# Kernel optimization log

Measured on AMD Instinct MI355X. Metric: run time of the kernel, lower is better.

## Reference

```python
import jax, jax.numpy as jnp
import numpy as np

N = 50000
E = 800000
DIMS = [128, 256, 64, 256, 128]  # encoder 128->256->64, decoder 64->256->128
NEG_SLOPE = 0.01


def setup_inputs() -> dict:
    key = jax.random.key(0)
    keys = jax.random.split(key, 2 + 3 * 4)
    inp = {
        "x": jax.random.normal(keys[0], (N, DIMS[0]), dtype=jnp.float32),
        "edge_index": jax.random.randint(keys[1], (2, E), 0, N, dtype=jnp.int64),
    }
    for i in range(4):
        d_in, d_out = DIMS[i], DIMS[i + 1]
        s = 1.0 / np.sqrt(d_in)
        inp[f"W_rel{i}"] = jax.random.uniform(keys[2 + 3 * i], (d_out, d_in), jnp.float32, -s, s)
        inp[f"W_root{i}"] = jax.random.uniform(keys[3 + 3 * i], (d_out, d_in), jnp.float32, -s, s)
        inp[f"b{i}"] = jax.random.uniform(keys[4 + 3 * i], (d_out,), jnp.float32, -s, s)
    return inp


def graph_conv(x, edge_index, W_rel, W_root, b):
    # PyG GraphConv: lin_rel(sum_{j->i} x_j) + lin_root(x_i), bias in lin_rel
    src, dst = edge_index[0], edge_index[1]
    agg = jax.ops.segment_sum(x[src], dst, num_segments=N)  # [N, d_in]
    return agg @ W_rel.T + b + x @ W_root.T


def reference(x, edge_index,
              W_rel0, W_root0, b0, W_rel1, W_root1, b1,
              W_rel2, W_root2, b2, W_rel3, W_root3, b3):
    params = [(W_rel0, W_root0, b0), (W_rel1, W_root1, b1),
              (W_rel2, W_root2, b2), (W_rel3, W_root3, b3)]
    h = x
    emb = None
    for i, (Wr, Ws, b) in enumerate(params):
        h = graph_conv(h, edge_index, Wr, Ws, b)
        h = jax.nn.leaky_relu(h, negative_slope=NEG_SLOPE)
        if i == 1:  # end of encoder -> embedding
            emb = h
    return h, emb
```

## Files before the change

### kernel.cpp

```cpp
#include <hip/hip_runtime.h>

#define NNODES 50000
#define NCB 196

typedef __attribute__((ext_vector_type(8))) short bf16x8;
typedef __attribute__((ext_vector_type(4))) float f32x4;

__device__ inline short f2bf(float f) {
    unsigned u = __float_as_uint(f);
    unsigned r = (u + 0x7FFFu + ((u >> 16) & 1u)) >> 16;
    return (short)r;
}
__device__ inline float bf2f(short s) {
    return __uint_as_float(((unsigned)(unsigned short)s) << 16);
}
__device__ inline float2 bfp2f(int p) {
    float2 f;
    f.x = __uint_as_float((unsigned)p << 16);
    f.y = __uint_as_float((unsigned)p & 0xFFFF0000u);
    return f;
}
__device__ inline void addbf4(float4& a, int2 v) {
    float2 lo = bfp2f(v.x), hi = bfp2f(v.y);
    a.x += lo.x; a.y += lo.y; a.z += hi.x; a.w += hi.y;
}
__device__ inline void addbf8(float* a, int4 v) {
    float2 l0 = bfp2f(v.x), l1 = bfp2f(v.y), l2 = bfp2f(v.z), l3 = bfp2f(v.w);
    a[0] += l0.x; a[1] += l0.y; a[2] += l1.x; a[3] += l1.y;
    a[4] += l2.x; a[5] += l2.y; a[6] += l3.x; a[7] += l3.y;
}
__device__ inline int pack2(float a, float b) {
    return ((int)(unsigned short)f2bf(a)) | ((int)f2bf(b) << 16);
}

__device__ inline int excl_scan_256(int v, int* lds, int tid) {
    int lane = tid & 63, w = tid >> 6;
    int incl = v;
    #pragma unroll
    for (int off = 1; off < 64; off <<= 1) {
        int t = __shfl_up(incl, off, 64);
        if (lane >= off) incl += t;
    }
    if (lane == 63) lds[w] = incl;
    __syncthreads();
    if (tid == 0) {
        int s = 0;
        #pragma unroll
        for (int i = 0; i < 4; i++) { int t = lds[i]; lds[i] = s; s += t; }
    }
    __syncthreads();
    return incl - v + lds[w];
}

__global__ __launch_bounds__(256) void hist_coarse(
    const int* __restrict__ dst, int* __restrict__ histG, int E, int chunk)
{
    __shared__ int h[NCB];
    const int tid = threadIdx.x;
    for (int i = tid; i < NCB; i += 256) h[i] = 0;
    __syncthreads();
    const int beg = blockIdx.x * chunk;
    const int end = min(beg + chunk, E);
    for (int e = beg + tid; e < end; e += 256)
        atomicAdd(&h[dst[e] >> 8], 1);
    __syncthreads();
    for (int i = tid; i < NCB; i += 256)
        histG[i * 256 + blockIdx.x] = h[i];
}

__global__ __launch_bounds__(256) void scan_buckets(
    int* __restrict__ histG, int* __restrict__ btot)
{
    __shared__ int lds[8];
    const int tid = threadIdx.x;
    const int b = blockIdx.x;
    int v = histG[b * 256 + tid];
    int ex = excl_scan_256(v, lds, tid);
    histG[b * 256 + tid] = ex;
    if (tid == 255) btot[b] = ex + v;
}

__global__ __launch_bounds__(256) void scan_bases(
    const int* __restrict__ btot, int* __restrict__ bases, int E)
{
    __shared__ int lds[8];
    const int tid = threadIdx.x;
    int v = (tid < NCB) ? btot[tid] : 0;
    int ex = excl_scan_256(v, lds, tid);
    if (tid <= NCB) bases[tid] = ex;
}

__global__ __launch_bounds__(256) void scatter_coarse(
    const int* __restrict__ src, const int* __restrict__ dst,
    const int* __restrict__ histG, const int* __restrict__ bases,
    int* __restrict__ coarse, int E, int chunk)
{
    __shared__ int pos[NCB];
    const int tid = threadIdx.x;
    const int blk = blockIdx.x;
    for (int i = tid; i < NCB; i += 256)
        pos[i] = bases[i] + histG[i * 256 + blk];
    __syncthreads();
    const int beg = blk * chunk;
    const int end = min(beg + chunk, E);
    for (int e = beg + tid; e < end; e += 256) {
        int d = dst[e];
        int p = atomicAdd(&pos[d >> 8], 1);
        coarse[p] = ((d & 255) << 16) | src[e];
    }
}

__global__ __launch_bounds__(256) void fill_from_coarse(
    const int* __restrict__ bases, const int* __restrict__ coarse,
    int* __restrict__ rowptr, int* __restrict__ col, int N)
{
    __shared__ int hist[256], rp[256], pos[256];
    __shared__ int lds[8];
    const int cb  = blockIdx.x;
    const int tid = threadIdx.x;
    const int n0  = cb << 8;
    const int beg = bases[cb], end = bases[cb + 1];
    hist[tid] = 0; pos[tid] = 0;
    __syncthreads();
    for (int e = beg + tid; e < end; e += 256)
        atomicAdd(&hist[coarse[e] >> 16], 1);
    __syncthreads();
    int ex = excl_scan_256(hist[tid], lds, tid);
    rp[tid] = beg + ex;
    if (n0 + tid <= N) rowptr[n0 + tid] = beg + ex;
    __syncthreads();
    for (int e = beg + tid; e < end; e += 256) {
        int pk = coarse[e];
        int dl = pk >> 16;
        int p = atomicAdd(&pos[dl], 1);
        col[rp[dl] + p] = pk & 0xFFFF;
    }
}

__global__ __launch_bounds__(256) void cvt_x(const float* __restrict__ in,
                                             short* __restrict__ out, int n4) {
    int i = blockIdx.x * 256 + threadIdx.x;
    if (i < n4) {
        float4 v = ((const float4*)in)[i];
        short4 s;
        s.x = f2bf(v.x); s.y = f2bf(v.y); s.z = f2bf(v.z); s.w = f2bf(v.w);
        *(short4*)(out + (size_t)i * 4) = s;
    }
}

__global__ __launch_bounds__(256) void cvt_weights(
    const float* __restrict__ p0, const float* __restrict__ p1,
    const float* __restrict__ p2, const float* __restrict__ p3,
    const float* __restrict__ p4, const float* __restrict__ p5,
    const float* __restrict__ p6, const float* __restrict__ p7,
    short* __restrict__ out) {
    int g = blockIdx.x * 256 + threadIdx.x;
    if (g >= 196608) return;
    const float* src; int off;
    if      (g <  32768) { src = p0; off = g; }
    else if (g <  65536) { src = p1; off = g -  32768; }
    else if (g <  81920) { src = p2; off = g -  65536; }
    else if (g <  98304) { src = p3; off = g -  81920; }
    else if (g < 114688) { src = p4; off = g -  98304; }
    else if (g < 131072) { src = p5; off = g - 114688; }
    else if (g < 163840) { src = p6; off = g - 131072; }
    else                 { src = p7; off = g - 163840; }
    out[g] = f2bf(src[off]);
}

__global__ __launch_bounds__(256) void gather_sum128(
    const short* __restrict__ xbf, const int* __restrict__ rowptr,
    const int* __restrict__ col, short* __restrict__ aggbf, int N)
{
    const int wave = threadIdx.x >> 6;
    const int lane = threadIdx.x & 63;
    const int node = blockIdx.x * 4 + wave;
    if (node >= N) return;
    const int g = lane >> 4;
    const int c = lane & 15;
    const int beg = rowptr[node], end = rowptr[node + 1];
    float acc[8] = {};
    const int last = end - 1;
    for (int e = beg; e < end; e += 16) {
        const int e0 = e + g, e1 = e + 4 + g, e2 = e + 8 + g, e3 = e + 12 + g;
        const bool m0 = e0 < end, m1 = e1 < end, m2 = e2 < end, m3 = e3 < end;
        const int i0 = col[min(e0, last)];
        const int i1 = col[min(e1, last)];
        const int i2 = col[min(e2, last)];
        const int i3 = col[min(e3, last)];
        int4 v0 = *(const int4*)(xbf + (size_t)i0 * 128 + c * 8);
        int4 v1 = *(const int4*)(xbf + (size_t)i1 * 128 + c * 8);
        int4 v2 = *(const int4*)(xbf + (size_t)i2 * 128 + c * 8);
        int4 v3 = *(const int4*)(xbf + (size_t)i3 * 128 + c * 8);
        if (m0) addbf8(acc, v0);
        if (m1) addbf8(acc, v1);
        if (m2) addbf8(acc, v2);
        if (m3) addbf8(acc, v3);
    }
    #pragma unroll
    for (int k = 0; k < 8; k++) acc[k] += __shfl_down(acc[k], 32);
    #pragma unroll
    for (int k = 0; k < 8; k++) acc[k] += __shfl_down(acc[k], 16);
    if (g == 0) {
        int4 sv;
        sv.x = pack2(acc[0], acc[1]);
        sv.y = pack2(acc[2], acc[3]);
        sv.z = pack2(acc[4], acc[5]);
        sv.w = pack2(acc[6], acc[7]);
        *(int4*)(aggbf + (size_t)node * 128 + c * 8) = sv;
    }
}

__global__ __launch_bounds__(256) void gather_sum64(
    const short* __restrict__ xbf, const int* __restrict__ rowptr,
    const int* __restrict__ col, short* __restrict__ aggbf, int N)
{
    const int wave = threadIdx.x >> 6;
    const int lane = threadIdx.x & 63;
    const int node = blockIdx.x * 4 + wave;
    if (node >= N) return;
    const int g = lane >> 3;
    const int c = lane & 7;
    const int beg = rowptr[node], end = rowptr[node + 1];
    float acc[8] = {};
    const int last = end - 1;
    for (int e = beg; e < end; e += 16) {
        const int e0 = e + g, e1 = e + 8 + g;
        const bool m0 = e0 < end, m1 = e1 < end;
        const int i0 = col[min(e0, last)];
        const int i1 = col[min(e1, last)];
        int4 v0 = *(const int4*)(xbf + (size_t)i0 * 64 + c * 8);
        int4 v1 = *(const int4*)(xbf + (size_t)i1 * 64 + c * 8);
        if (m0) addbf8(acc, v0);
        if (m1) addbf8(acc, v1);
    }
    #pragma unroll
    for (int k = 0; k < 8; k++) acc[k] += __shfl_down(acc[k], 32);
    #pragma unroll
    for (int k = 0; k < 8; k++) acc[k] += __shfl_down(acc[k], 16);
    #pragma unroll
    for (int k = 0; k < 8; k++) acc[k] += __shfl_down(acc[k], 8);
    if (g == 0) {
        int4 sv;
        sv.x = pack2(acc[0], acc[1]);
        sv.y = pack2(acc[2], acc[3]);
        sv.z = pack2(acc[4], acc[5]);
        sv.w = pack2(acc[6], acc[7]);
        *(int4*)(aggbf + (size_t)node * 64 + c * 8) = sv;
    }
}

__global__ __launch_bounds__(256) void gather_fin128(
    const short* __restrict__ zw, const int* __restrict__ rowptr,
    const int* __restrict__ col, const float* __restrict__ bias,
    float* __restrict__ out, int N)
{
    const int wave = threadIdx.x >> 6;
    const int lane = threadIdx.x & 63;
    const int node = blockIdx.x * 4 + wave;
    if (node >= N) return;
    const int g = lane >> 4;
    const int c = lane & 15;
    const int beg = rowptr[node], end = rowptr[node + 1];
    float acc[8] = {};
    if (g == 0) {
        int4 wv = *(const int4*)(zw + (size_t)node * 256 + 128 + c * 8);
        addbf8(acc, wv);
        float4 b0 = *(const float4*)(bias + c * 8);
        float4 b1 = *(const float4*)(bias + c * 8 + 4);
        acc[0] += b0.x; acc[1] += b0.y; acc[2] += b0.z; acc[3] += b0.w;
        acc[4] += b1.x; acc[5] += b1.y; acc[6] += b1.z; acc[7] += b1.w;
    }
    const int last = end - 1;
    for (int e = beg; e < end; e += 16) {
        const int e0 = e + g, e1 = e + 4 + g, e2 = e + 8 + g, e3 = e + 12 + g;
        const bool m0 = e0 < end, m1 = e1 < end, m2 = e2 < end, m3 = e3 < end;
        const int i0 = col[min(e0, last)];
        const int i1 = col[min(e1, last)];
        const int i2 = col[min(e2, last)];
        const int i3 = col[min(e3, last)];
        int4 v0 = *(const int4*)(zw + (size_t)i0 * 256 + c * 8);
        int4 v1 = *(const int4*)(zw + (size_t)i1 * 256 + c * 8);
        int4 v2 = *(const int4*)(zw + (size_t)i2 * 256 + c * 8);
        int4 v3 = *(const int4*)(zw + (size_t)i3 * 256 + c * 8);
        if (m0) addbf8(acc, v0);
        if (m1) addbf8(acc, v1);
        if (m2) addbf8(acc, v2);
        if (m3) addbf8(acc, v3);
    }
    #pragma unroll
    for (int k = 0; k < 8; k++) acc[k] += __shfl_down(acc[k], 32);
    #pragma unroll
    for (int k = 0; k < 8; k++) acc[k] += __shfl_down(acc[k], 16);
    if (g == 0) {
        #pragma unroll
        for (int k = 0; k < 8; k++) acc[k] = acc[k] > 0.f ? acc[k] : 0.01f * acc[k];
        float4 o0 = make_float4(acc[0], acc[1], acc[2], acc[3]);
        float4 o1 = make_float4(acc[4], acc[5], acc[6], acc[7]);
        *(float4*)(out + (size_t)node * 128 + c * 8)     = o0;
        *(float4*)(out + (size_t)node * 128 + c * 8 + 4) = o1;
    }
}

__global__ __launch_bounds__(256) void gather_fin64(
    const short* __restrict__ zw, const int* __restrict__ rowptr,
    const int* __restrict__ col, const float* __restrict__ bias,
    float* __restrict__ out, short* __restrict__ out_bf, int N)
{
    const int wave = threadIdx.x >> 6;
    const int lane = threadIdx.x & 63;
    const int node = blockIdx.x * 4 + wave;
    if (node >= N) return;
    const int g = lane >> 3;
    const int c = lane & 7;
    const int beg = rowptr[node], end = rowptr[node + 1];
    float acc[8] = {};
    if (g == 0) {
        int4 wv = *(const int4*)(zw + (size_t)node * 128 + 64 + c * 8);
        addbf8(acc, wv);
        float4 b0 = *(const float4*)(bias + c * 8);
        float4 b1 = *(const float4*)(bias + c * 8 + 4);
        acc[0] += b0.x; acc[1] += b0.y; acc[2] += b0.z; acc[3] += b0.w;
        acc[4] += b1.x; acc[5] += b1.y; acc[6] += b1.z; acc[7] += b1.w;
    }
    const int last = end - 1;
    for (int e = beg; e < end; e += 16) {
        const int e0 = e + g, e1 = e + 8 + g;
        const bool m0 = e0 < end, m1 = e1 < end;
        const int i0 = col[min(e0, last)];
        const int i1 = col[min(e1, last)];
        int4 v0 = *(const int4*)(zw + (size_t)i0 * 128 + c * 8);
        int4 v1 = *(const int4*)(zw + (size_t)i1 * 128 + c * 8);
        if (m0) addbf8(acc, v0);
        if (m1) addbf8(acc, v1);
    }
    #pragma unroll
    for (int k = 0; k < 8; k++) acc[k] += __shfl_down(acc[k], 32);
    #pragma unroll
    for (int k = 0; k < 8; k++) acc[k] += __shfl_down(acc[k], 16);
    #pragma unroll
    for (int k = 0; k < 8; k++) acc[k] += __shfl_down(acc[k], 8);
    if (g == 0) {
        #pragma unroll
        for (int k = 0; k < 8; k++) acc[k] = acc[k] > 0.f ? acc[k] : 0.01f * acc[k];
        float4 o0 = make_float4(acc[0], acc[1], acc[2], acc[3]);
        float4 o1 = make_float4(acc[4], acc[5], acc[6], acc[7]);
        *(float4*)(out + (size_t)node * 64 + c * 8)     = o0;
        *(float4*)(out + (size_t)node * 64 + c * 8 + 4) = o1;
        int4 sv;
        sv.x = pack2(acc[0], acc[1]);
        sv.y = pack2(acc[2], acc[3]);
        sv.z = pack2(acc[4], acc[5]);
        sv.w = pack2(acc[6], acc[7]);
        *(int4*)(out_bf + (size_t)node * 64 + c * 8) = sv;
    }
}

template<int DK, int DOUT, bool FUSED>
__global__ __launch_bounds__(256) void gemm_mfma(
    const short* __restrict__ A0, const short* __restrict__ A1,
    const short* __restrict__ B0, const short* __restrict__ B1,
    const float* __restrict__ bias, short* __restrict__ outH, int N)
{
    constexpr int KTOT  = FUSED ? 2 * DK : DK;
    constexpr int NCOLS = FUSED ? DOUT : 2 * DOUT;
    constexpr int K32   = KTOT / 32;
    constexpr int KSEG  = KTOT / 8;
    constexpr int BSH   = 128 * KTOT;
    constexpr int SMSH  = (BSH > 18432) ? BSH : 18432;

    __shared__ short smem[SMSH];
    const int tid  = threadIdx.x;
    const int row0 = blockIdx.x * 128;
    const int col0 = blockIdx.y * 128;
    const int w    = tid >> 6;
    const int lane = tid & 63;
    const int wr   = (w & 1) << 6;
    const int wc   = (w >> 1) << 6;
    const int m16  = lane & 15;
    const int quad = lane >> 4;

    #pragma unroll
    for (int it = 0; it < BSH / 8 / 256; it++) {
        int idx = tid + it * 256;
        int j = idx / KSEG;
        int t = idx % KSEG;
        int gj = col0 + j;
        const short* bp;
        int ko = t * 8;
        if (FUSED) {
            if (ko < DK) bp = B0 + (size_t)gj * DK + ko;
            else         bp = B1 + (size_t)gj * DK + (ko - DK);
        } else {
            bp = (gj < DOUT) ? (B0 + (size_t)gj * DK + ko)
                             : (B1 + (size_t)(gj - DOUT) * DK + ko);
        }
        int4 v = *(const int4*)bp;
        int kk = t >> 2, qd = t & 3, jj = j >> 4, mm = j & 15;
        *(int4*)(smem + ((((jj * K32 + kk) * 4 + qd) * 16 + mm) << 3)) = v;
    }
    __syncthreads();

    const short* arow[4];
    #pragma unroll
    for (int i = 0; i < 4; i++) {
        int r = row0 + wr + i * 16 + m16;
        r = r < N ? r : N - 1;
        arow[i] = A0 + (size_t)r * DK;
    }
    const size_t a1delta = (size_t)(A1 - A0);

    f32x4 acc[4][4] = {};
    const int jw = wc >> 4;

    #pragma unroll
    for (int kk = 0; kk < K32; kk++) {
        const int ko = kk * 32;
        bf16x8 af[4];
        #pragma unroll
        for (int i = 0; i < 4; i++) {
            const short* ap = arow[i] + (quad << 3);
            if (FUSED && ko >= DK) ap += a1delta + (ko - DK);
            else                   ap += ko;
            af[i] = *(const bf16x8*)ap;
        }
        #pragma unroll
        for (int j = 0; j < 4; j++) {
            bf16x8 bfr = *(const bf16x8*)(smem +
                (((((jw + j) * K32 + kk) * 4 + quad) * 16 + m16) << 3));
            #pragma unroll
            for (int i = 0; i < 4; i++)
                acc[i][j] = __builtin_amdgcn_mfma_f32_16x16x32_bf16(
                    af[i], bfr, acc[i][j], 0, 0, 0);
        }
    }

    __syncthreads();
    short* ep = smem + w * 4608;
    #pragma unroll
    for (int j = 0; j < 4; j++) {
        const int colg = col0 + wc + j * 16 + m16;
        const float bv = FUSED ? bias[colg] : 0.f;
        #pragma unroll
        for (int i = 0; i < 4; i++) {
            #pragma unroll
            for (int r = 0; r < 4; r++) {
                float v = acc[i][j][r];
                if (FUSED) { v += bv; v = v > 0.f ? v : 0.01f * v; }
                ep[(i * 16 + quad * 4 + r) * 72 + j * 16 + m16] = f2bf(v);
            }
        }
    }
    const int r8  = lane >> 3;
    const int seg = lane & 7;
    #pragma unroll
    for (int rb = 0; rb < 8; rb++) {
        const int lrow = rb * 8 + r8;
        int4 vv = *(const int4*)(ep + lrow * 72 + seg * 8);
        const int grow = row0 + wr + lrow;
        if (grow < N)
            *(int4*)(outH + (size_t)grow * NCOLS + col0 + wc + seg * 8) = vv;
    }
}

extern "C" void kernel_launch(void* const* d_in, const int* in_sizes, int n_in,
                              void* d_out, int out_size, void* d_ws, size_t ws_size,
                              hipStream_t stream) {
    const int N = NNODES;
    const float* x  = (const float*)d_in[0];
    const int*   ei = (const int*)d_in[1];
    const int    E  = in_sizes[1] / 2;
    const int* src = ei;
    const int* dst = ei + E;

    const float* Wr[4] = { (const float*)d_in[2], (const float*)d_in[5],
                           (const float*)d_in[8], (const float*)d_in[11] };
    const float* Ws[4] = { (const float*)d_in[3], (const float*)d_in[6],
                           (const float*)d_in[9], (const float*)d_in[12] };
    const float* bb[4] = { (const float*)d_in[4], (const float*)d_in[7],
                           (const float*)d_in[10], (const float*)d_in[13] };

    float* out  = (float*)d_out;
    float* emb  = out + (size_t)N * 128;

    short* zwbf   = (short*)d_ws;
    short* aggbf  = zwbf + (size_t)N * 256;
    short* xbf    = aggbf + (size_t)N * 128;
    short* h1bf   = xbf + (size_t)N * 128;
    short* embbf  = h1bf + (size_t)N * 256;
    short* wbf    = embbf + (size_t)N * 64;
    int*   rowptr = (int*)(wbf + 196608);
    int*   col    = rowptr + (N + 1);
    int*   coarse = col + E;
    int*   histG  = coarse + E;
    int*   btot   = histG + NCB * 256;
    int*   bases  = btot + NCB;

    const short* wr0 = wbf;           const short* ws0 = wbf + 32768;
    const short* wr1 = wbf + 65536;   const short* ws1 = wbf + 81920;
    const short* wr2 = wbf + 98304;   const short* ws2 = wbf + 114688;
    const short* wr3 = wbf + 131072;  const short* ws3 = wbf + 163840;

    const int chunk = (E + 255) / 256;
    const int gemmRB = (N + 127) / 128;
    const int nodeBlocks = (N + 3) / 4;

    hist_coarse<<<256, 256, 0, stream>>>(dst, histG, E, chunk);
    scan_buckets<<<NCB, 256, 0, stream>>>(histG, btot);
    scan_bases<<<1, 256, 0, stream>>>(btot, bases, E);
    scatter_coarse<<<256, 256, 0, stream>>>(src, dst, histG, bases, coarse, E, chunk);
    fill_from_coarse<<<NCB, 256, 0, stream>>>(bases, coarse, rowptr, col, N);
    cvt_x<<<(N * 128 / 4 + 255) / 256, 256, 0, stream>>>(x, xbf, N * 128 / 4);
    cvt_weights<<<(196608 + 255) / 256, 256, 0, stream>>>(
        Wr[0], Ws[0], Wr[1], Ws[1], Wr[2], Ws[2], Wr[3], Ws[3], wbf);

    gather_sum128<<<nodeBlocks, 256, 0, stream>>>(xbf, rowptr, col, aggbf, N);
    gemm_mfma<128, 256, true><<<dim3(gemmRB, 2), 256, 0, stream>>>(
        aggbf, xbf, wr0, ws0, bb[0], h1bf, N);

    gemm_mfma<256, 64, false><<<dim3(gemmRB, 1), 256, 0, stream>>>(
        h1bf, nullptr, wr1, ws1, nullptr, zwbf, N);
    gather_fin64<<<nodeBlocks, 256, 0, stream>>>(
        zwbf, rowptr, col, bb[1], emb, embbf, N);

    gather_sum64<<<nodeBlocks, 256, 0, stream>>>(embbf, rowptr, col, aggbf, N);
    gemm_mfma<64, 256, true><<<dim3(gemmRB, 2), 256, 0, stream>>>(
        aggbf, embbf, wr2, ws2, bb[2], h1bf , N);

    gemm_mfma<256, 128, false><<<dim3(gemmRB, 2), 256, 0, stream>>>(
        h1bf , nullptr, wr3, ws3, nullptr, zwbf, N);
    gather_fin128<<<nodeBlocks, 256, 0, stream>>>(
        zwbf, rowptr, col, bb[3], out, N);
}
```

Measured before the change: 330.0 us.

## Load GEMM weights via global_load_lds and cover all output columns per block

The GEMM kernel now stages the whole weight matrix into LDS with direct global-to-LDS loads instead of register round-trips. It drops the column-block grid dimension, so each 128-row block uses 8 warps to cover every output column and the A rows are read once. The MFMA operands are swapped so each lane holds 4 consecutive output columns, which lets the epilogue write packed bf16 straight to global memory without the LDS transpose and extra barrier. The trade-offs are larger LDS use per block (up to 128KB), larger blocks that may lower occupancy, and narrower 8-byte global stores.

```diff
diff --git a/kernel.cpp b/kernel.cpp
--- a/kernel.cpp
+++ b/kernel.cpp
@@ -5,6 +5,9 @@
 
 typedef __attribute__((ext_vector_type(8))) short bf16x8;
 typedef __attribute__((ext_vector_type(4))) float f32x4;
+
+#define AS1 __attribute__((address_space(1)))
+#define AS3 __attribute__((address_space(3)))
 
 __device__ inline short f2bf(float f) {
     unsigned u = __float_as_uint(f);
@@ -356,23 +359,23 @@
     }
 }
 
-template<int DK, int DOUT, bool FUSED>
-__global__ __launch_bounds__(256) void gemm_mfma(
+template<int DK, int DOUT, bool FUSED, int NW>
+__global__ __launch_bounds__(NW * 64) void gemm_mfma(
     const short* __restrict__ A0, const short* __restrict__ A1,
     const short* __restrict__ B0, const short* __restrict__ B1,
     const float* __restrict__ bias, short* __restrict__ outH, int N)
 {
     constexpr int KTOT  = FUSED ? 2 * DK : DK;
     constexpr int NCOLS = FUSED ? DOUT : 2 * DOUT;
+    constexpr int NT    = NW * 64;
     constexpr int K32   = KTOT / 32;
-    constexpr int KSEG  = KTOT / 8;
-    constexpr int BSH   = 128 * KTOT;
-    constexpr int SMSH  = (BSH > 18432) ? BSH : 18432;
-
-    __shared__ short smem[SMSH];
+    constexpr int LOG2K32 = (K32 == 8) ? 3 : 2;
+    constexpr int BINT4 = NCOLS * KTOT / 8;
+    constexpr int ITER  = BINT4 / NT;
+
+    __shared__ short smem[NCOLS * KTOT];
     const int tid  = threadIdx.x;
     const int row0 = blockIdx.x * 128;
-    const int col0 = blockIdx.y * 128;
     const int w    = tid >> 6;
     const int lane = tid & 63;
     const int wr   = (w & 1) << 6;
@@ -381,23 +384,24 @@
     const int quad = lane >> 4;
 
     #pragma unroll
-    for (int it = 0; it < BSH / 8 / 256; it++) {
-        int idx = tid + it * 256;
-        int j = idx / KSEG;
-        int t = idx % KSEG;
-        int gj = col0 + j;
+    for (int it = 0; it < ITER; it++) {
+        const int L  = tid + it * NT;
+        const int mm = L & 15;
+        const int qd = (L >> 4) & 3;
+        const int kk = (L >> 6) & (K32 - 1);
+        const int jj = L >> (6 + LOG2K32);
+        const int j  = jj * 16 + mm;
+        const int ko = (kk * 4 + qd) * 8;
         const short* bp;
-        int ko = t * 8;
         if (FUSED) {
-            if (ko < DK) bp = B0 + (size_t)gj * DK + ko;
-            else         bp = B1 + (size_t)gj * DK + (ko - DK);
+            if (ko < DK) bp = B0 + (size_t)j * DK + ko;
+            else         bp = B1 + (size_t)j * DK + (ko - DK);
         } else {
-            bp = (gj < DOUT) ? (B0 + (size_t)gj * DK + ko)
-                             : (B1 + (size_t)(gj - DOUT) * DK + ko);
+            bp = (j < DOUT) ? (B0 + (size_t)j * DK + ko)
+                            : (B1 + (size_t)(j - DOUT) * DK + ko);
         }
-        int4 v = *(const int4*)bp;
-        int kk = t >> 2, qd = t & 3, jj = j >> 4, mm = j & 15;
-        *(int4*)(smem + ((((jj * K32 + kk) * 4 + qd) * 16 + mm) << 3)) = v;
+        __builtin_amdgcn_global_load_lds(
+            (const AS1 void*)bp, (AS3 void*)(smem + ((size_t)L << 3)), 16, 0, 0);
     }
     __syncthreads();
 
@@ -408,7 +412,7 @@
         r = r < N ? r : N - 1;
         arow[i] = A0 + (size_t)r * DK;
     }
-    const size_t a1delta = (size_t)(A1 - A0);
+    const size_t a1delta = FUSED ? (size_t)(A1 - A0) : 0;
 
     f32x4 acc[4][4] = {};
     const int jw = wc >> 4;
@@ -431,35 +435,33 @@
             #pragma unroll
             for (int i = 0; i < 4; i++)
                 acc[i][j] = __builtin_amdgcn_mfma_f32_16x16x32_bf16(
-                    af[i], bfr, acc[i][j], 0, 0, 0);
+                    bfr, af[i], acc[i][j], 0, 0, 0);
         }
     }
 
-    __syncthreads();
-    short* ep = smem + w * 4608;
     #pragma unroll
     for (int j = 0; j < 4; j++) {
-        const int colg = col0 + wc + j * 16 + m16;
-        const float bv = FUSED ? bias[colg] : 0.f;
+        const int cb = wc + j * 16 + (quad << 2);
+        float4 bv = make_float4(0.f, 0.f, 0.f, 0.f);
+        if (FUSED) bv = *(const float4*)(bias + cb);
         #pragma unroll
         for (int i = 0; i < 4; i++) {
-            #pragma unroll
-            for (int r = 0; r < 4; r++) {
-                float v = acc[i][j][r];
-                if (FUSED) { v += bv; v = v > 0.f ? v : 0.01f * v; }
-                ep[(i * 16 + quad * 4 + r) * 72 + j * 16 + m16] = f2bf(v);
+            const int grow = row0 + wr + i * 16 + m16;
+            float v0 = acc[i][j][0], v1 = acc[i][j][1];
+            float v2 = acc[i][j][2], v3 = acc[i][j][3];
+            if (FUSED) {
+                v0 += bv.x; v1 += bv.y; v2 += bv.z; v3 += bv.w;
+                v0 = v0 > 0.f ? v0 : 0.01f * v0;
+                v1 = v1 > 0.f ? v1 : 0.01f * v1;
+                v2 = v2 > 0.f ? v2 : 0.01f * v2;
+                v3 = v3 > 0.f ? v3 : 0.01f * v3;
             }
+            int2 sv;
+            sv.x = pack2(v0, v1);
+            sv.y = pack2(v2, v3);
+            if (grow < N)
+                *(int2*)(outH + (size_t)grow * NCOLS + cb) = sv;
         }
-    }
-    const int r8  = lane >> 3;
-    const int seg = lane & 7;
-    #pragma unroll
-    for (int rb = 0; rb < 8; rb++) {
-        const int lrow = rb * 8 + r8;
-        int4 vv = *(const int4*)(ep + lrow * 72 + seg * 8);
-        const int grow = row0 + wr + lrow;
-        if (grow < N)
-            *(int4*)(outH + (size_t)grow * NCOLS + col0 + wc + seg * 8) = vv;
     }
 }
 
@@ -515,19 +517,19 @@
         Wr[0], Ws[0], Wr[1], Ws[1], Wr[2], Ws[2], Wr[3], Ws[3], wbf);
 
     gather_sum128<<<nodeBlocks, 256, 0, stream>>>(xbf, rowptr, col, aggbf, N);
-    gemm_mfma<128, 256, true><<<dim3(gemmRB, 2), 256, 0, stream>>>(
+    gemm_mfma<128, 256, true, 8><<<gemmRB, 512, 0, stream>>>(
         aggbf, xbf, wr0, ws0, bb[0], h1bf, N);
 
-    gemm_mfma<256, 64, false><<<dim3(gemmRB, 1), 256, 0, stream>>>(
+    gemm_mfma<256, 64, false, 4><<<gemmRB, 256, 0, stream>>>(
         h1bf, nullptr, wr1, ws1, nullptr, zwbf, N);
     gather_fin64<<<nodeBlocks, 256, 0, stream>>>(
         zwbf, rowptr, col, bb[1], emb, embbf, N);
 
     gather_sum64<<<nodeBlocks, 256, 0, stream>>>(embbf, rowptr, col, aggbf, N);
-    gemm_mfma<64, 256, true><<<dim3(gemmRB, 2), 256, 0, stream>>>(
+    gemm_mfma<64, 256, true, 8><<<gemmRB, 512, 0, stream>>>(
         aggbf, embbf, wr2, ws2, bb[2], h1bf , N);
 
-    gemm_mfma<256, 128, false><<<dim3(gemmRB, 2), 256, 0, stream>>>(
+    gemm_mfma<256, 128, false, 8><<<gemmRB, 512, 0, stream>>>(
         h1bf , nullptr, wr3, ws3, nullptr, zwbf, N);
     gather_fin128<<<nodeBlocks, 256, 0, stream>>>(
         zwbf, rowptr, col, bb[3], out, N);
```

Result: slower. 349.5 us (+5.9%).

## Load GEMM weight fragments directly from global memory, drop LDS staging

Applied to the files above, without the earlier changes.

The MFMA GEMM no longer stages the whole weight tile into shared memory with a block-wide barrier. Each lane now reads its B fragments straight from global (cache-resident) memory. The MFMA operands are swapped so the accumulator is transposed, which lets the epilogue pack four contiguous columns into one int2 store and load the bias as a float4. Shared memory shrinks to the epilogue buffer only, and launch bounds request 4 blocks per CU for occupancy, at the cost of more global/L2 traffic for weights.

```diff
diff --git a/kernel.cpp b/kernel.cpp
--- a/kernel.cpp
+++ b/kernel.cpp
@@ -357,7 +357,7 @@
 }
 
 template<int DK, int DOUT, bool FUSED>
-__global__ __launch_bounds__(256) void gemm_mfma(
+__global__ __launch_bounds__(256, 4) void gemm_mfma(
     const short* __restrict__ A0, const short* __restrict__ A1,
     const short* __restrict__ B0, const short* __restrict__ B1,
     const float* __restrict__ bias, short* __restrict__ outH, int N)
@@ -365,11 +365,8 @@
     constexpr int KTOT  = FUSED ? 2 * DK : DK;
     constexpr int NCOLS = FUSED ? DOUT : 2 * DOUT;
     constexpr int K32   = KTOT / 32;
-    constexpr int KSEG  = KTOT / 8;
-    constexpr int BSH   = 128 * KTOT;
-    constexpr int SMSH  = (BSH > 18432) ? BSH : 18432;
-
-    __shared__ short smem[SMSH];
+
+    __shared__ short eps[4 * 4608];
     const int tid  = threadIdx.x;
     const int row0 = blockIdx.x * 128;
     const int col0 = blockIdx.y * 128;
@@ -380,38 +377,31 @@
     const int m16  = lane & 15;
     const int quad = lane >> 4;
 
-    #pragma unroll
-    for (int it = 0; it < BSH / 8 / 256; it++) {
-        int idx = tid + it * 256;
-        int j = idx / KSEG;
-        int t = idx % KSEG;
-        int gj = col0 + j;
-        const short* bp;
-        int ko = t * 8;
-        if (FUSED) {
-            if (ko < DK) bp = B0 + (size_t)gj * DK + ko;
-            else         bp = B1 + (size_t)gj * DK + (ko - DK);
-        } else {
-            bp = (gj < DOUT) ? (B0 + (size_t)gj * DK + ko)
-                             : (B1 + (size_t)(gj - DOUT) * DK + ko);
-        }
-        int4 v = *(const int4*)bp;
-        int kk = t >> 2, qd = t & 3, jj = j >> 4, mm = j & 15;
-        *(int4*)(smem + ((((jj * K32 + kk) * 4 + qd) * 16 + mm) << 3)) = v;
-    }
-    __syncthreads();
-
     const short* arow[4];
     #pragma unroll
     for (int i = 0; i < 4; i++) {
         int r = row0 + wr + i * 16 + m16;
         r = r < N ? r : N - 1;
-        arow[i] = A0 + (size_t)r * DK;
-    }
-    const size_t a1delta = (size_t)(A1 - A0);
+        arow[i] = A0 + (size_t)r * DK + (quad << 3);
+    }
+    const size_t a1d = FUSED ? (size_t)(A1 - A0) : 0;
+
+    const short* blo[4];
+    const short* bhi[4];
+    #pragma unroll
+    for (int j = 0; j < 4; j++) {
+        const int cg = col0 + wc + j * 16 + m16;
+        if (FUSED) {
+            blo[j] = B0 + (size_t)cg * DK + (quad << 3);
+            bhi[j] = B1 + (size_t)cg * DK + (quad << 3);
+        } else {
+            blo[j] = ((cg < DOUT) ? (B0 + (size_t)cg * DK)
+                                  : (B1 + (size_t)(cg - DOUT) * DK)) + (quad << 3);
+            bhi[j] = blo[j];
+        }
+    }
 
     f32x4 acc[4][4] = {};
-    const int jw = wc >> 4;
 
     #pragma unroll
     for (int kk = 0; kk < K32; kk++) {
@@ -419,36 +409,45 @@
         bf16x8 af[4];
         #pragma unroll
         for (int i = 0; i < 4; i++) {
-            const short* ap = arow[i] + (quad << 3);
-            if (FUSED && ko >= DK) ap += a1delta + (ko - DK);
+            const short* ap = arow[i];
+            if (FUSED && ko >= DK) ap += a1d + (ko - DK);
             else                   ap += ko;
             af[i] = *(const bf16x8*)ap;
         }
         #pragma unroll
         for (int j = 0; j < 4; j++) {
-            bf16x8 bfr = *(const bf16x8*)(smem +
-                (((((jw + j) * K32 + kk) * 4 + quad) * 16 + m16) << 3));
+            const short* bp;
+            if (FUSED && ko >= DK) bp = bhi[j] + (ko - DK);
+            else                   bp = blo[j] + ko;
+            bf16x8 bfr = *(const bf16x8*)bp;
             #pragma unroll
             for (int i = 0; i < 4; i++)
                 acc[i][j] = __builtin_amdgcn_mfma_f32_16x16x32_bf16(
-                    af[i], bfr, acc[i][j], 0, 0, 0);
+                    bfr, af[i], acc[i][j], 0, 0, 0);
         }
     }
 
-    __syncthreads();
-    short* ep = smem + w * 4608;
+    short* ep = eps + w * 4608;
     #pragma unroll
     for (int j = 0; j < 4; j++) {
-        const int colg = col0 + wc + j * 16 + m16;
-        const float bv = FUSED ? bias[colg] : 0.f;
+        const int cb = wc + j * 16 + (quad << 2);
+        float4 bv = make_float4(0.f, 0.f, 0.f, 0.f);
+        if (FUSED) bv = *(const float4*)(bias + col0 + cb);
         #pragma unroll
         for (int i = 0; i < 4; i++) {
-            #pragma unroll
-            for (int r = 0; r < 4; r++) {
-                float v = acc[i][j][r];
-                if (FUSED) { v += bv; v = v > 0.f ? v : 0.01f * v; }
-                ep[(i * 16 + quad * 4 + r) * 72 + j * 16 + m16] = f2bf(v);
+            float v0 = acc[i][j][0], v1 = acc[i][j][1];
+            float v2 = acc[i][j][2], v3 = acc[i][j][3];
+            if (FUSED) {
+                v0 += bv.x; v1 += bv.y; v2 += bv.z; v3 += bv.w;
+                v0 = v0 > 0.f ? v0 : 0.01f * v0;
+                v1 = v1 > 0.f ? v1 : 0.01f * v1;
+                v2 = v2 > 0.f ? v2 : 0.01f * v2;
+                v3 = v3 > 0.f ? v3 : 0.01f * v3;
             }
+            int2 pv;
+            pv.x = pack2(v0, v1);
+            pv.y = pack2(v2, v3);
+            *(int2*)(ep + (i * 16 + m16) * 72 + j * 16 + (quad << 2)) = pv;
         }
     }
     const int r8  = lane >> 3;
```

New measurement: 359.6 us. 1.09x slower.
